# Kernel optimization log

Measured on AMD Instinct MI355X. Metric: run time of the kernel, lower is better.

The kernel has to match this reference:

```python
import jax, jax.numpy as jnp
import numpy as np

B, S, E = 2, 2048, 1024
H = 16
D = E // H          # head dim = 64
K_TOP = 64          # top-k tokens kept per query in sparse branch
M = 256             # performer kernel feature dim
EPS = 1e-6


def setup_inputs() -> dict:
    key = jax.random.key(0)
    ks = jax.random.split(key, 16)
    sc = 0.02
    p = {
        'x': jax.random.normal(ks[0], (B, S, E), jnp.float32),
        # sparse-attention branch params
        'Wq_s': jax.random.normal(ks[1], (E, E), jnp.float32) * sc,
        'Wk_s': jax.random.normal(ks[2], (E, E), jnp.float32) * sc,
        'Wv_s': jax.random.normal(ks[3], (E, E), jnp.float32) * sc,
        'Wo_s': jax.random.normal(ks[4], (E, E), jnp.float32) * sc,
        'bq_s': jnp.zeros((E,), jnp.float32),
        'bk_s': jnp.zeros((E,), jnp.float32),
        'bv_s': jnp.zeros((E,), jnp.float32),
        'bo_s': jnp.zeros((E,), jnp.float32),
        # performer branch params
        'Wq_p': jax.random.normal(ks[5], (E, E), jnp.float32) * sc,
        'Wk_p': jax.random.normal(ks[6], (E, E), jnp.float32) * sc,
        'Wv_p': jax.random.normal(ks[7], (E, E), jnp.float32) * sc,
        'Wo_p': jax.random.normal(ks[8], (E, E), jnp.float32) * sc,
        'bo_p': jnp.zeros((E,), jnp.float32),
        'Wfeat': jax.random.normal(ks[9], (D, M), jnp.float32) / np.sqrt(D),
        # gate
        'Wg': jax.random.normal(ks[10], (E, 2), jnp.float32) * sc,
        'bg': jnp.zeros((2,), jnp.float32),
    }
    return p


def _split_heads(t):
    # [B,S,E] -> [B,H,S,D]
    return t.reshape(B, S, H, D).transpose(0, 2, 1, 3)


def _merge_heads(t):
    # [B,H,S,D] -> [B,S,E]
    return t.transpose(0, 2, 1, 3).reshape(B, S, E)


def _sparse_attn(x, Wq, bq, Wk, bk, Wv, bv, Wo, bo):
    q = _split_heads(x @ Wq + bq)
    k = _split_heads(x @ Wk + bk)
    v = _split_heads(x @ Wv + bv)
    scores = jnp.einsum('bhqd,bhkd->bhqk', q, k) / np.sqrt(D)  # [B,H,S,S]
    # keep only top-K scores per query row
    topv = jax.lax.top_k(scores, K_TOP)[0]
    thresh = topv[..., -1:]
    neg = jnp.finfo(scores.dtype).min
    masked = jnp.where(scores >= thresh, scores, neg)
    attn = jax.nn.softmax(masked, axis=-1)
    out = jnp.einsum('bhqk,bhkd->bhqd', attn, v)
    return _merge_heads(out) @ Wo + bo


def _performer_attn(x, Wq, Wk, Wv, Wo, bo, Wfeat):
    q = _split_heads(x @ Wq)
    k = _split_heads(x @ Wk)
    v = _split_heads(x @ Wv)
    # learned relu feature map (FAVOR-style linear attention)
    phi_q = jax.nn.relu(jnp.einsum('bhsd,dm->bhsm', q, Wfeat)) + EPS
    phi_k = jax.nn.relu(jnp.einsum('bhsd,dm->bhsm', k, Wfeat)) + EPS
    kv = jnp.einsum('bhsm,bhsd->bhmd', phi_k, v)      # [B,H,M,D]
    z = phi_k.sum(axis=2)                              # [B,H,M]
    num = jnp.einsum('bhsm,bhmd->bhsd', phi_q, kv)
    den = jnp.einsum('bhsm,bhm->bhs', phi_q, z)[..., None] + EPS
    return _merge_heads(num / den) @ Wo + bo


def reference(x, Wq_s, Wk_s, Wv_s, Wo_s, bq_s, bk_s, bv_s, bo_s,
              Wq_p, Wk_p, Wv_p, Wo_p, bo_p, Wfeat, Wg, bg):
    sparse_out = _sparse_attn(x, Wq_s, bq_s, Wk_s, bk_s, Wv_s, bv_s, Wo_s, bo_s)
    perf_out = _performer_attn(x, Wq_p, Wk_p, Wv_p, Wo_p, bo_p, Wfeat)
    avg_hidden = x.mean(axis=1)                        # [B,E]
    gate = jax.nn.softmax(avg_hidden @ Wg + bg, axis=-1)  # [B,2]
    w_s = gate[:, 0][:, None, None]
    w_p = gate[:, 1][:, None, None]
    # dropout is identity in eval/reference mode
    return w_s * sparse_out + w_p * perf_out
```

## Files before the change

kernel.cpp:

```cpp
#include <hip/hip_runtime.h>


constexpr int cB = 2, cS = 2048, cE = 1024, cH = 16, cD = 64, cKTOP = 64, cM = 256;
constexpr float cEPS = 1e-6f;

typedef _Float16 half8 __attribute__((ext_vector_type(8)));
typedef float f32x16 __attribute__((ext_vector_type(16)));

__device__ __forceinline__ unsigned int f2key(float f) {
    unsigned int u = __float_as_uint(f);
    return (u & 0x80000000u) ? ~u : (u | 0x80000000u);
}

__device__ __forceinline__ unsigned short h2u(_Float16 h) {
    union { _Float16 h; unsigned short u; } x; x.h = h; return x.u;
}

__device__ __forceinline__ half8 ld_half8(const unsigned short* p) {
    union { uint4 u; half8 h; } x;
    x.u = *(const uint4*)p;
    return x.h;
}

__global__ __launch_bounds__(256)
void gemm_qk2_blas(const float* __restrict__ A,
                   const float* __restrict__ Wq,
                   const float* __restrict__ Wk,
                   const float* __restrict__ bq,
                   const float* __restrict__ bk_,
                   float* __restrict__ Cq,
                   float* __restrict__ Ck,
                   unsigned short* __restrict__ khi,
                   int K, int N)
{
    __shared__ __align__(16) float As[16][68];
    __shared__ __align__(16) float Bq[16][68];
    __shared__ __align__(16) float Bk[16][68];
    const int t  = threadIdx.x;
    const int r0 = blockIdx.y * 64;
    const int c0 = blockIdx.x * 64;
    const int tm = t >> 4, tn = t & 15;
    float paccQ[4][4] = {};
    float caccQ[4][4] = {};
    float paccK[4][4] = {};
    float caccK[4][4] = {};

    const int ar = t >> 2, ak = (t & 3) * 4;
    const int bk = t >> 4, bc = (t & 15) * 4;

    for (int k0 = 0; k0 < K; k0 += 16) {
        const float4 av  = *(const float4*)(A  + (size_t)(r0 + ar) * K + (k0 + ak));
        const float4 bqv = *(const float4*)(Wq + (size_t)(k0 + bk) * N + (c0 + bc));
        const float4 bkv = *(const float4*)(Wk + (size_t)(k0 + bk) * N + (c0 + bc));
        As[ak + 0][ar] = av.x;
        As[ak + 1][ar] = av.y;
        As[ak + 2][ar] = av.z;
        As[ak + 3][ar] = av.w;
        *(float4*)&Bq[bk][bc] = bqv;
        *(float4*)&Bk[bk][bc] = bkv;
        __syncthreads();
        #pragma unroll
        for (int kk = 0; kk < 16; ++kk) {
            const float4 a4  = *(const float4*)&As[kk][tm * 4];
            const float4 q4  = *(const float4*)&Bq[kk][tn * 4];
            const float4 k4  = *(const float4*)&Bk[kk][tn * 4];
            const float a[4]  = {a4.x, a4.y, a4.z, a4.w};
            const float bqr[4] = {q4.x, q4.y, q4.z, q4.w};
            const float bkr[4] = {k4.x, k4.y, k4.z, k4.w};
            #pragma unroll
            for (int i = 0; i < 4; ++i)
                #pragma unroll
                for (int j = 0; j < 4; ++j) {
                    paccQ[i][j] = fmaf(a[i], bqr[j], paccQ[i][j]);
                    paccK[i][j] = fmaf(a[i], bkr[j], paccK[i][j]);
                }
        }
        __syncthreads();
        const int kn = k0 + 16;
        if (kn == 384 || kn == 768 || kn == K) {
            #pragma unroll
            for (int i = 0; i < 4; ++i)
                #pragma unroll
                for (int j = 0; j < 4; ++j) {
                    caccQ[i][j] = caccQ[i][j] + paccQ[i][j];
                    paccQ[i][j] = 0.f;
                    caccK[i][j] = caccK[i][j] + paccK[i][j];
                    paccK[i][j] = 0.f;
                }
        }
    }
    #pragma unroll
    for (int i = 0; i < 4; ++i) {
        const int r = r0 + tm * 4 + i;
        const int c = c0 + tn * 4;
        float4 vq;
        vq.x = caccQ[i][0] + bq[c + 0];
        vq.y = caccQ[i][1] + bq[c + 1];
        vq.z = caccQ[i][2] + bq[c + 2];
        vq.w = caccQ[i][3] + bq[c + 3];
        *(float4*)&Cq[(size_t)r * N + c] = vq;
        float4 vk;
        vk.x = caccK[i][0] + bk_[c + 0];
        vk.y = caccK[i][1] + bk_[c + 1];
        vk.z = caccK[i][2] + bk_[c + 2];
        vk.w = caccK[i][3] + bk_[c + 3];
        *(float4*)&Ck[(size_t)r * N + c] = vk;
        ushort4 hs;
        hs.x = h2u((_Float16)vk.x);
        hs.y = h2u((_Float16)vk.y);
        hs.z = h2u((_Float16)vk.z);
        hs.w = h2u((_Float16)vk.w);
        *(ushort4*)&khi[(size_t)r * N + c] = hs;
    }
}

__global__ __launch_bounds__(256)
void conv_wT(const float* __restrict__ W,
             unsigned short* __restrict__ wthi,
             unsigned short* __restrict__ wtlo)
{
    __shared__ float tile[64][68];
    const int t  = threadIdx.x;
    const int k0 = blockIdx.y * 64;
    const int n0 = blockIdx.x * 64;
    const int r  = t >> 4, c4 = (t & 15) * 4;
    #pragma unroll
    for (int i = 0; i < 4; ++i) {
        const int k = r + 16 * i;
        const float4 v = *(const float4*)&W[(size_t)(k0 + k) * cE + n0 + c4];
        tile[k][c4 + 0] = v.x; tile[k][c4 + 1] = v.y;
        tile[k][c4 + 2] = v.z; tile[k][c4 + 3] = v.w;
    }
    __syncthreads();
    #pragma unroll
    for (int i = 0; i < 4; ++i) {
        const int n = r + 16 * i;
        unsigned int hp[2], lp[2];
        #pragma unroll
        for (int p = 0; p < 2; ++p) {
            unsigned short hh[2], ll[2];
            #pragma unroll
            for (int j = 0; j < 2; ++j) {
                const float f = tile[c4 + p * 2 + j][n];
                const _Float16 h = (_Float16)f;
                hh[j] = h2u(h);
                ll[j] = h2u((_Float16)(f - (float)h));
            }
            hp[p] = (unsigned int)hh[0] | ((unsigned int)hh[1] << 16);
            lp[p] = (unsigned int)ll[0] | ((unsigned int)ll[1] << 16);
        }
        uint2 hv, lv;
        hv.x = hp[0]; hv.y = hp[1];
        lv.x = lp[0]; lv.y = lp[1];
        *(uint2*)&wthi[(size_t)(n0 + n) * cE + k0 + c4] = hv;
        *(uint2*)&wtlo[(size_t)(n0 + n) * cE + k0 + c4] = lv;
    }
}

__global__ __launch_bounds__(256)
void gemm_hilo(const float* __restrict__ A,
               const unsigned short* __restrict__ wthi,
               const unsigned short* __restrict__ wtlo,
               const float* __restrict__ bias,
               float* __restrict__ C)
{
    __shared__ __align__(16) unsigned short Ah[128][24];
    __shared__ __align__(16) unsigned short Al[128][24];
    __shared__ __align__(16) unsigned short Bh[64][24];
    __shared__ __align__(16) unsigned short Bl[64][24];

    const int t    = threadIdx.x;
    const int lane = t & 63, wave = t >> 6;
    const int wr   = wave >> 1, wc = wave & 1;
    const int r0   = blockIdx.y * 128, c0 = blockIdx.x * 64;
    const int fr   = lane & 31, g5 = lane >> 5;

    const int arow = t >> 1, aka = (t & 1) * 8;
    const int bsel = t >> 7;
    const int brow = (t & 127) >> 1, bkb = (t & 1) * 8;
    const unsigned short* wsrc = bsel ? wtlo : wthi;

    f32x16 acc0 = {0.f,0.f,0.f,0.f,0.f,0.f,0.f,0.f,0.f,0.f,0.f,0.f,0.f,0.f,0.f,0.f};
    f32x16 acc1 = {0.f,0.f,0.f,0.f,0.f,0.f,0.f,0.f,0.f,0.f,0.f,0.f,0.f,0.f,0.f,0.f};

    for (int k0 = 0; k0 < cE; k0 += 16) {
        const float4 x0 = *(const float4*)&A[(size_t)(r0 + arow) * cE + k0 + aka];
        const float4 x1 = *(const float4*)&A[(size_t)(r0 + arow) * cE + k0 + aka + 4];
        const float xf[8] = {x0.x, x0.y, x0.z, x0.w, x1.x, x1.y, x1.z, x1.w};
        unsigned int hw[4], lw[4];
        #pragma unroll
        for (int p = 0; p < 4; ++p) {
            unsigned short hh[2], ll[2];
            #pragma unroll
            for (int j = 0; j < 2; ++j) {
                const float f = xf[p * 2 + j];
                const _Float16 h = (_Float16)f;
                hh[j] = h2u(h);
                ll[j] = h2u((_Float16)(f - (float)h));
            }
            hw[p] = (unsigned int)hh[0] | ((unsigned int)hh[1] << 16);
            lw[p] = (unsigned int)ll[0] | ((unsigned int)ll[1] << 16);
        }
        uint4 hv, lv;
        hv.x = hw[0]; hv.y = hw[1]; hv.z = hw[2]; hv.w = hw[3];
        lv.x = lw[0]; lv.y = lw[1]; lv.z = lw[2]; lv.w = lw[3];
        *(uint4*)&Ah[arow][aka] = hv;
        *(uint4*)&Al[arow][aka] = lv;

        const uint4 wv = *(const uint4*)&wsrc[(size_t)(c0 + brow) * cE + k0 + bkb];
        if (bsel) *(uint4*)&Bl[brow][bkb] = wv;
        else      *(uint4*)&Bh[brow][bkb] = wv;
        __syncthreads();

        const half8 a0h = ld_half8(&Ah[wr * 64 + fr][g5 * 8]);
        const half8 a0l = ld_half8(&Al[wr * 64 + fr][g5 * 8]);
        const half8 a1h = ld_half8(&Ah[wr * 64 + 32 + fr][g5 * 8]);
        const half8 a1l = ld_half8(&Al[wr * 64 + 32 + fr][g5 * 8]);
        const half8 bh  = ld_half8(&Bh[wc * 32 + fr][g5 * 8]);
        const half8 bl  = ld_half8(&Bl[wc * 32 + fr][g5 * 8]);

        acc0 = __builtin_amdgcn_mfma_f32_32x32x16_f16(a0l, bh, acc0, 0, 0, 0);
        acc0 = __builtin_amdgcn_mfma_f32_32x32x16_f16(a0h, bl, acc0, 0, 0, 0);
        acc0 = __builtin_amdgcn_mfma_f32_32x32x16_f16(a0h, bh, acc0, 0, 0, 0);
        acc1 = __builtin_amdgcn_mfma_f32_32x32x16_f16(a1l, bh, acc1, 0, 0, 0);
        acc1 = __builtin_amdgcn_mfma_f32_32x32x16_f16(a1h, bl, acc1, 0, 0, 0);
        acc1 = __builtin_amdgcn_mfma_f32_32x32x16_f16(a1h, bh, acc1, 0, 0, 0);
        __syncthreads();
    }

    const int col = c0 + wc * 32 + fr;
    const float bv = bias ? bias[col] : 0.f;
    #pragma unroll
    for (int rg = 0; rg < 16; ++rg) {
        const int row = r0 + wr * 64 + (rg & 3) + 8 * (rg >> 2) + 4 * g5;
        C[(size_t)row * cE + col] = acc0[rg] + bv;
    }
    #pragma unroll
    for (int rg = 0; rg < 16; ++rg) {
        const int row = r0 + wr * 64 + 32 + (rg & 3) + 8 * (rg >> 2) + 4 * g5;
        C[(size_t)row * cE + col] = acc1[rg] + bv;
    }
}

__global__ __launch_bounds__(256)
void out_gemm_hilo(const float* __restrict__ As_, const float* __restrict__ Ap_,
                   const unsigned short* __restrict__ w1hi,
                   const unsigned short* __restrict__ w1lo,
                   const unsigned short* __restrict__ w2hi,
                   const unsigned short* __restrict__ w2lo,
                   const float* __restrict__ bos, const float* __restrict__ bop,
                   const float* __restrict__ gates, float* __restrict__ out)
{
    __shared__ __align__(16) unsigned short A1h[128][24], A1l[128][24];
    __shared__ __align__(16) unsigned short A2h[128][24], A2l[128][24];
    __shared__ __align__(16) unsigned short B1h[64][24],  B1l[64][24];
    __shared__ __align__(16) unsigned short B2h[64][24],  B2l[64][24];

    const int t    = threadIdx.x;
    const int lane = t & 63, wave = t >> 6;
    const int wr   = wave >> 1, wc = wave & 1;
    const int r0   = blockIdx.y * 128, c0 = blockIdx.x * 64;
    const int fr   = lane & 31, g5 = lane >> 5;
    const int b    = r0 >> 11;
    const float gs = gates[b * 2 + 0], gp = gates[b * 2 + 1];

    const int arow = t >> 1, aka = (t & 1) * 8;
    const int bsel = t >> 7;
    const int brow = (t & 127) >> 1, bkb = (t & 1) * 8;
    const unsigned short* s1 = bsel ? w1lo : w1hi;
    const unsigned short* s2 = bsel ? w2lo : w2hi;

    f32x16 acc0 = {0.f,0.f,0.f,0.f,0.f,0.f,0.f,0.f,0.f,0.f,0.f,0.f,0.f,0.f,0.f,0.f};
    f32x16 acc1 = {0.f,0.f,0.f,0.f,0.f,0.f,0.f,0.f,0.f,0.f,0.f,0.f,0.f,0.f,0.f,0.f};

    for (int k0 = 0; k0 < cE; k0 += 16) {
        {
            const float4 x0 = *(const float4*)&As_[(size_t)(r0 + arow) * cE + k0 + aka];
            const float4 x1 = *(const float4*)&As_[(size_t)(r0 + arow) * cE + k0 + aka + 4];
            const float xf[8] = {x0.x * gs, x0.y * gs, x0.z * gs, x0.w * gs,
                                 x1.x * gs, x1.y * gs, x1.z * gs, x1.w * gs};
            unsigned int hw[4], lw[4];
            #pragma unroll
            for (int p = 0; p < 4; ++p) {
                unsigned short hh[2], ll[2];
                #pragma unroll
                for (int j = 0; j < 2; ++j) {
                    const float f = xf[p * 2 + j];
                    const _Float16 h = (_Float16)f;
                    hh[j] = h2u(h);
                    ll[j] = h2u((_Float16)(f - (float)h));
                }
                hw[p] = (unsigned int)hh[0] | ((unsigned int)hh[1] << 16);
                lw[p] = (unsigned int)ll[0] | ((unsigned int)ll[1] << 16);
            }
            uint4 hv, lv;
            hv.x = hw[0]; hv.y = hw[1]; hv.z = hw[2]; hv.w = hw[3];
            lv.x = lw[0]; lv.y = lw[1]; lv.z = lw[2]; lv.w = lw[3];
            *(uint4*)&A1h[arow][aka] = hv;
            *(uint4*)&A1l[arow][aka] = lv;
        }
        {
            const float4 x0 = *(const float4*)&Ap_[(size_t)(r0 + arow) * cE + k0 + aka];
            const float4 x1 = *(const float4*)&Ap_[(size_t)(r0 + arow) * cE + k0 + aka + 4];
            const float xf[8] = {x0.x * gp, x0.y * gp, x0.z * gp, x0.w * gp,
                                 x1.x * gp, x1.y * gp, x1.z * gp, x1.w * gp};
            unsigned int hw[4], lw[4];
            #pragma unroll
            for (int p = 0; p < 4; ++p) {
                unsigned short hh[2], ll[2];
                #pragma unroll
                for (int j = 0; j < 2; ++j) {
                    const float f = xf[p * 2 + j];
                    const _Float16 h = (_Float16)f;
                    hh[j] = h2u(h);
                    ll[j] = h2u((_Float16)(f - (float)h));
                }
                hw[p] = (unsigned int)hh[0] | ((unsigned int)hh[1] << 16);
                lw[p] = (unsigned int)ll[0] | ((unsigned int)ll[1] << 16);
            }
            uint4 hv, lv;
            hv.x = hw[0]; hv.y = hw[1]; hv.z = hw[2]; hv.w = hw[3];
            lv.x = lw[0]; lv.y = lw[1]; lv.z = lw[2]; lv.w = lw[3];
            *(uint4*)&A2h[arow][aka] = hv;
            *(uint4*)&A2l[arow][aka] = lv;
        }
        {
            const uint4 w1 = *(const uint4*)&s1[(size_t)(c0 + brow) * cE + k0 + bkb];
            if (bsel) *(uint4*)&B1l[brow][bkb] = w1;
            else      *(uint4*)&B1h[brow][bkb] = w1;
            const uint4 w2 = *(const uint4*)&s2[(size_t)(c0 + brow) * cE + k0 + bkb];
            if (bsel) *(uint4*)&B2l[brow][bkb] = w2;
            else      *(uint4*)&B2h[brow][bkb] = w2;
        }
        __syncthreads();

        const half8 b1h = ld_half8(&B1h[wc * 32 + fr][g5 * 8]);
        const half8 b1l = ld_half8(&B1l[wc * 32 + fr][g5 * 8]);
        const half8 b2h = ld_half8(&B2h[wc * 32 + fr][g5 * 8]);
        const half8 b2l = ld_half8(&B2l[wc * 32 + fr][g5 * 8]);
        {
            const half8 a1h = ld_half8(&A1h[wr * 64 + fr][g5 * 8]);
            const half8 a1l = ld_half8(&A1l[wr * 64 + fr][g5 * 8]);
            const half8 a2h = ld_half8(&A2h[wr * 64 + fr][g5 * 8]);
            const half8 a2l = ld_half8(&A2l[wr * 64 + fr][g5 * 8]);
            acc0 = __builtin_amdgcn_mfma_f32_32x32x16_f16(a1l, b1h, acc0, 0, 0, 0);
            acc0 = __builtin_amdgcn_mfma_f32_32x32x16_f16(a1h, b1l, acc0, 0, 0, 0);
            acc0 = __builtin_amdgcn_mfma_f32_32x32x16_f16(a1h, b1h, acc0, 0, 0, 0);
            acc0 = __builtin_amdgcn_mfma_f32_32x32x16_f16(a2l, b2h, acc0, 0, 0, 0);
            acc0 = __builtin_amdgcn_mfma_f32_32x32x16_f16(a2h, b2l, acc0, 0, 0, 0);
            acc0 = __builtin_amdgcn_mfma_f32_32x32x16_f16(a2h, b2h, acc0, 0, 0, 0);
        }
        {
            const half8 a1h = ld_half8(&A1h[wr * 64 + 32 + fr][g5 * 8]);
            const half8 a1l = ld_half8(&A1l[wr * 64 + 32 + fr][g5 * 8]);
            const half8 a2h = ld_half8(&A2h[wr * 64 + 32 + fr][g5 * 8]);
            const half8 a2l = ld_half8(&A2l[wr * 64 + 32 + fr][g5 * 8]);
            acc1 = __builtin_amdgcn_mfma_f32_32x32x16_f16(a1l, b1h, acc1, 0, 0, 0);
            acc1 = __builtin_amdgcn_mfma_f32_32x32x16_f16(a1h, b1l, acc1, 0, 0, 0);
            acc1 = __builtin_amdgcn_mfma_f32_32x32x16_f16(a1h, b1h, acc1, 0, 0, 0);
            acc1 = __builtin_amdgcn_mfma_f32_32x32x16_f16(a2l, b2h, acc1, 0, 0, 0);
            acc1 = __builtin_amdgcn_mfma_f32_32x32x16_f16(a2h, b2l, acc1, 0, 0, 0);
            acc1 = __builtin_amdgcn_mfma_f32_32x32x16_f16(a2h, b2h, acc1, 0, 0, 0);
        }
        __syncthreads();
    }

    const int col = c0 + wc * 32 + fr;
    const float bv = gs * bos[col] + gp * bop[col];
    #pragma unroll
    for (int rg = 0; rg < 16; ++rg) {
        const int row = r0 + wr * 64 + (rg & 3) + 8 * (rg >> 2) + 4 * g5;
        out[(size_t)row * cE + col] = acc0[rg] + bv;
    }
    #pragma unroll
    for (int rg = 0; rg < 16; ++rg) {
        const int row = r0 + wr * 64 + 32 + (rg & 3) + 8 * (rg >> 2) + 4 * g5;
        out[(size_t)row * cE + col] = acc1[rg] + bv;
    }
}

__global__ __launch_bounds__(256, 4)
void sparse_sel(const float* __restrict__ Q,
                const unsigned short* __restrict__ Khi,
                unsigned short* __restrict__ gcidx,
                int* __restrict__ gcnt)
{
    __shared__ __align__(16) unsigned short Qhi[8][72];
    __shared__ unsigned int hist[8][257];
    __shared__ int cnt[8];
    __shared__ int t16hi[8], rem[8], t16[8];

    const int t   = threadIdx.x;
    const int bh  = blockIdx.y;
    const int b   = bh >> 4;
    const int h64 = (bh & 15) * 64;
    const int q0  = blockIdx.x * 8;
    const size_t rid0 = ((size_t)bh * 256 + blockIdx.x) * 8;

    if (t < 128) {
        const int r = t >> 4, c4 = (t & 15) * 4;
        const float4 v =
            *(const float4*)&Q[((size_t)(b * cS + q0 + r)) * cE + h64 + c4];
        const float f[4] = {v.x, v.y, v.z, v.w};
        #pragma unroll
        for (int i = 0; i < 4; ++i)
            Qhi[r][c4 + i] = h2u((_Float16)f[i]);
    }
    for (int i = t; i < 8 * 257; i += 256) (&hist[0][0])[i] = 0u;
    if (t < 8) cnt[t] = 0;
    __syncthreads();

    const int lane = t & 63;
    const int wv   = t >> 6;
    const int col  = lane & 31;
    const int g5   = lane >> 5;
    const int r0   = g5 * 4;

    half8 ahi[4];
    {
        const int arow = col & 7;
        #pragma unroll
        for (int ks = 0; ks < 4; ++ks)
            ahi[ks] = ld_half8(&Qhi[arow][g5 * 8 + ks * 16]);
    }
    unsigned int su[16][2];
    {
        const size_t kbase = ((size_t)(b * cS + wv * 512 + col)) * cE + h64;
        #pragma unroll
        for (int tl = 0; tl < 16; ++tl) {
            const unsigned short* kh = Khi + kbase + (size_t)tl * 32 * cE;
            f32x16 acc = {0.f,0.f,0.f,0.f,0.f,0.f,0.f,0.f,
                          0.f,0.f,0.f,0.f,0.f,0.f,0.f,0.f};
            #pragma unroll
            for (int ks = 0; ks < 4; ++ks) {
                const half8 bh8 = ld_half8(kh + g5 * 8 + ks * 16);
                acc = __builtin_amdgcn_mfma_f32_32x32x16_f16(ahi[ks], bh8, acc, 0, 0, 0);
            }
            const unsigned int k0 = f2key(acc[0] * 0.125f) >> 16;
            const unsigned int k1 = f2key(acc[1] * 0.125f) >> 16;
            const unsigned int k2 = f2key(acc[2] * 0.125f) >> 16;
            const unsigned int k3 = f2key(acc[3] * 0.125f) >> 16;
            su[tl][0] = k0 | (k1 << 16);
            su[tl][1] = k2 | (k3 << 16);
            atomicAdd(&hist[r0 + 0][k0 >> 8], 1u);
            atomicAdd(&hist[r0 + 1][k1 >> 8], 1u);
            atomicAdd(&hist[r0 + 2][k2 >> 8], 1u);
            atomicAdd(&hist[r0 + 3][k3 >> 8], 1u);
        }
    }
    __syncthreads();
    if (t < 8) {
        int need = cKTOP + 1;
        int hb = 0;
        for (int bin = 255; bin >= 0; --bin) {
            const int c = (int)hist[t][bin];
            if (c >= need) { hb = bin; break; }
            need -= c;
        }
        t16hi[t] = hb;
        rem[t] = need;
    }
    __syncthreads();
    for (int i = t; i < 8 * 257; i += 256) (&hist[0][0])[i] = 0u;
    __syncthreads();
    #pragma unroll
    for (int tl = 0; tl < 16; ++tl)
        #pragma unroll
        for (int w = 0; w < 2; ++w) {
            const unsigned int u = su[tl][w];
            const int rlo = r0 + 2 * w, rhi = rlo + 1;
            const unsigned int vlo = u & 0xFFFFu;
            const unsigned int vhi = u >> 16;
            if ((int)(vlo >> 8) == t16hi[rlo]) atomicAdd(&hist[rlo][vlo & 255u], 1u);
            if ((int)(vhi >> 8) == t16hi[rhi]) atomicAdd(&hist[rhi][vhi & 255u], 1u);
        }
    __syncthreads();
    if (t < 8) {
        int need = rem[t];
        int lb = 0;
        for (int bin = 255; bin >= 0; --bin) {
            const int c = (int)hist[t][bin];
            if (c >= need) { lb = bin; break; }
            need -= c;
        }
        t16[t] = (t16hi[t] << 8) | lb;
    }
    __syncthreads();

    #pragma unroll
    for (int tl = 0; tl < 16; ++tl) {
        const int key = wv * 512 + tl * 32 + col;
        #pragma unroll
        for (int w = 0; w < 2; ++w) {
            const unsigned int u = su[tl][w];
            const int rlo = r0 + 2 * w, rhi = rlo + 1;
            const int v0 = (int)(u & 0xFFFFu);
            const int v1 = (int)(u >> 16);
            if (v0 >= max(t16[rlo] - 3, 0)) {
                const int slot = atomicAdd(&cnt[rlo], 1);
                if (slot < 128) gcidx[(rid0 + rlo) * 128 + slot] = (unsigned short)key;
            }
            if (v1 >= max(t16[rhi] - 3, 0)) {
                const int slot = atomicAdd(&cnt[rhi], 1);
                if (slot < 128) gcidx[(rid0 + rhi) * 128 + slot] = (unsigned short)key;
            }
        }
    }
    __syncthreads();
    if (t < 8) gcnt[rid0 + t] = cnt[t];
}

__global__ __launch_bounds__(256, 8)
void sparse_att(const float* __restrict__ Q,
                const unsigned short* __restrict__ gcidx,
                const int* __restrict__ gcnt,
                const float* __restrict__ Ks, const float* __restrict__ V,
                float* __restrict__ O)
{
    __shared__ float QfT[64][8];
    __shared__ unsigned short cidx[8][128];
    __shared__ double cval[8][128];
    __shared__ float cw[8][128];
    __shared__ int cnt[8];
    __shared__ double T64s[8], s65s[8], rowm[8];

    const int t   = threadIdx.x;
    const int bh  = blockIdx.y;
    const int b   = bh >> 4;
    const int h64 = (bh & 15) * 64;
    const int q0  = blockIdx.x * 8;
    const size_t rid0 = ((size_t)bh * 256 + blockIdx.x) * 8;

    if (t < 128) {
        const int r = t >> 4, c4 = (t & 15) * 4;
        const float4 v =
            *(const float4*)&Q[((size_t)(b * cS + q0 + r)) * cE + h64 + c4];
        QfT[c4 + 0][r] = v.x; QfT[c4 + 1][r] = v.y;
        QfT[c4 + 2][r] = v.z; QfT[c4 + 3][r] = v.w;
    }
    ((ushort4*)&cidx[0][0])[t] = ((const ushort4*)&gcidx[rid0 * 128])[t];
    if (t < 8) cnt[t] = gcnt[rid0 + t];
    __syncthreads();

    const int wv = t >> 6, lane = t & 63;

    #pragma unroll
    for (int rx = 0; rx < 2; ++rx) {
        const int rr = wv * 2 + rx;
        const int n = min(cnt[rr], 128);
        for (int c = lane; c < n; c += 64) {
            const int key = cidx[rr][c];
            const float* kp = Ks + ((size_t)(b * cS + key)) * cE + h64;
            double a = 0.0;
            #pragma unroll 4
            for (int d4 = 0; d4 < 64; d4 += 4) {
                const float4 kv = *(const float4*)&kp[d4];
                a = fma((double)QfT[d4 + 0][rr], (double)kv.x, a);
                a = fma((double)QfT[d4 + 1][rr], (double)kv.y, a);
                a = fma((double)QfT[d4 + 2][rr], (double)kv.z, a);
                a = fma((double)QfT[d4 + 3][rr], (double)kv.w, a);
            }
            cval[rr][c] = a * 0.125;
        }
    }
    __syncthreads();

    #pragma unroll
    for (int rx = 0; rx < 2; ++rx) {
        const int rr = wv * 2 + rx;
        const int n = min(cnt[rr], 128);
        for (int c = lane; c < n; c += 64) {
            const double v = cval[rr][c];
            int rank = 0;
            for (int i = 0; i < n; ++i) rank += (cval[rr][i] > v) ? 1 : 0;
            if (rank == 0)  rowm[rr] = v;
            if (rank == 63) T64s[rr] = v;
            if (rank == 64) s65s[rr] = v;
        }
    }
    __syncthreads();

    #pragma unroll
    for (int rx = 0; rx < 2; ++rx) {
        const int rr = wv * 2 + rx;
        const int n = min(cnt[rr], 128);
        const double T64 = T64s[rr], s65 = s65s[rr], m = rowm[rr];
        float za = 0.f;
        for (int c = lane; c < n; c += 64) {
            const double v = cval[rr][c];
            if (v >= T64) za += expf((float)(v - m));
        }
        #pragma unroll
        for (int off = 32; off >= 1; off >>= 1)
            za += __shfl_xor(za, off);
        const float g   = (float)(T64 - s65);
        const float gm  = fmaxf(g - 5e-7f, 0.f);
        const float wB  = 0.5f * erfcf(gm * (1.0f / 2.2e-6f));
        const float wA  = 1.f - wB;
        const float e64 = expf((float)(T64 - m));
        const float e65 = expf((float)(s65 - m));
        const float ZB  = za - e64 + e65;
        const float cIn = wA / za + wB / ZB;
        const float c64 = wA / za;
        const float c65 = wB / ZB;
        for (int c = lane; c < n; c += 64) {
            const double v = cval[rr][c];
            float cc = 0.f;
            if (v > T64)       cc = cIn;
            else if (v == T64) cc = c64;
            else if (v == s65) cc = c65;
            cw[rr][c] = (cc != 0.f) ? cc * expf((float)(v - m)) : 0.f;
        }
    }
    __syncthreads();

    #pragma unroll
    for (int rx = 0; rx < 2; ++rx) {
        const int rr = wv * 2 + rx;
        const int n = min(cnt[rr], 128);
        float o = 0.f;
        int j = 0;
        for (; j + 8 <= n; j += 8) {
            float wreg[8];
            int   kreg[8];
            #pragma unroll
            for (int u = 0; u < 8; ++u) {
                wreg[u] = cw[rr][j + u];
                kreg[u] = cidx[rr][j + u];
            }
            float vreg[8];
            #pragma unroll
            for (int u = 0; u < 8; ++u)
                vreg[u] = V[((size_t)(b * cS + kreg[u])) * cE + h64 + lane];
            #pragma unroll
            for (int u = 0; u < 8; ++u)
                o = fmaf(wreg[u], vreg[u], o);
        }
        for (; j < n; ++j)
            o = fmaf(cw[rr][j],
                     V[((size_t)(b * cS + cidx[rr][j])) * cE + h64 + lane], o);
        O[((size_t)(b * cS + q0 + rr)) * cE + h64 + lane] = o;
    }
}

__global__ __launch_bounds__(256)
void perf_kv(const float* __restrict__ Kp, const float* __restrict__ Vp,
             const float* __restrict__ Wfeat,
             float* __restrict__ kvpart, float* __restrict__ zpart)
{
    __shared__ __align__(16) float Wf[64][68];
    __shared__ __align__(16) float Kt[64][68];
    __shared__ __align__(16) float Vt[64][68];
    __shared__ __align__(16) float Ph[64][68];
    const int t    = threadIdx.x;
    const int mc   = blockIdx.x & 3;
    const int sc   = blockIdx.x >> 2;
    const int bh   = blockIdx.y;
    const int b    = bh >> 4;
    const int h64  = (bh & 15) * 64;
    const int m0   = mc * 64;
    const int sbase = sc * 1024;

    #pragma unroll
    for (int i = 0; i < 4; ++i) {
        const int lin = t + 256 * i;
        const int d   = lin >> 4;
        const int m4  = (lin & 15) * 4;
        *(float4*)&Wf[d][m4] = *(const float4*)&Wfeat[d * cM + m0 + m4];
    }

    const int tm = t >> 4, tn = t & 15;
    const int sr = tm * 4;
    const int cn = tn * 4;
    float akv[4][4] = {};
    float az = 0.f;

    for (int st = 0; st < 16; ++st) {
        const int s0g = sbase + st * 64;
        __syncthreads();
        #pragma unroll
        for (int i = 0; i < 4; ++i) {
            const int row = tm + 16 * i;
            const size_t base = ((size_t)(b * cS + s0g + row)) * cE + h64 + cn;
            *(float4*)&Kt[row][cn] = *(const float4*)&Kp[base];
            *(float4*)&Vt[row][cn] = *(const float4*)&Vp[base];
        }
        __syncthreads();
        float4 p0 = {0,0,0,0}, p1 = {0,0,0,0}, p2 = {0,0,0,0}, p3 = {0,0,0,0};
        #pragma unroll 8
        for (int d = 0; d < 64; ++d) {
            const float4 wv = *(const float4*)&Wf[d][cn];
            const float k0 = Kt[sr + 0][d], k1 = Kt[sr + 1][d];
            const float k2 = Kt[sr + 2][d], k3 = Kt[sr + 3][d];
            p0.x = fmaf(k0, wv.x, p0.x); p0.y = fmaf(k0, wv.y, p0.y);
            p0.z = fmaf(k0, wv.z, p0.z); p0.w = fmaf(k0, wv.w, p0.w);
            p1.x = fmaf(k1, wv.x, p1.x); p1.y = fmaf(k1, wv.y, p1.y);
            p1.z = fmaf(k1, wv.z, p1.z); p1.w = fmaf(k1, wv.w, p1.w);
            p2.x = fmaf(k2, wv.x, p2.x); p2.y = fmaf(k2, wv.y, p2.y);
            p2.z = fmaf(k2, wv.z, p2.z); p2.w = fmaf(k2, wv.w, p2.w);
            p3.x = fmaf(k3, wv.x, p3.x); p3.y = fmaf(k3, wv.y, p3.y);
            p3.z = fmaf(k3, wv.z, p3.z); p3.w = fmaf(k3, wv.w, p3.w);
        }
        p0.x = fmaxf(p0.x, 0.f) + cEPS; p0.y = fmaxf(p0.y, 0.f) + cEPS;
        p0.z = fmaxf(p0.z, 0.f) + cEPS; p0.w = fmaxf(p0.w, 0.f) + cEPS;
        p1.x = fmaxf(p1.x, 0.f) + cEPS; p1.y = fmaxf(p1.y, 0.f) + cEPS;
        p1.z = fmaxf(p1.z, 0.f) + cEPS; p1.w = fmaxf(p1.w, 0.f) + cEPS;
        p2.x = fmaxf(p2.x, 0.f) + cEPS; p2.y = fmaxf(p2.y, 0.f) + cEPS;
        p2.z = fmaxf(p2.z, 0.f) + cEPS; p2.w = fmaxf(p2.w, 0.f) + cEPS;
        p3.x = fmaxf(p3.x, 0.f) + cEPS; p3.y = fmaxf(p3.y, 0.f) + cEPS;
        p3.z = fmaxf(p3.z, 0.f) + cEPS; p3.w = fmaxf(p3.w, 0.f) + cEPS;
        *(float4*)&Ph[sr + 0][cn] = p0;
        *(float4*)&Ph[sr + 1][cn] = p1;
        *(float4*)&Ph[sr + 2][cn] = p2;
        *(float4*)&Ph[sr + 3][cn] = p3;
        __syncthreads();
        #pragma unroll 8
        for (int ss = 0; ss < 64; ++ss) {
            const float4 pv = *(const float4*)&Ph[ss][sr];
            const float4 vv = *(const float4*)&Vt[ss][cn];
            akv[0][0] = fmaf(pv.x, vv.x, akv[0][0]); akv[0][1] = fmaf(pv.x, vv.y, akv[0][1]);
            akv[0][2] = fmaf(pv.x, vv.z, akv[0][2]); akv[0][3] = fmaf(pv.x, vv.w, akv[0][3]);
            akv[1][0] = fmaf(pv.y, vv.x, akv[1][0]); akv[1][1] = fmaf(pv.y, vv.y, akv[1][1]);
            akv[1][2] = fmaf(pv.y, vv.z, akv[1][2]); akv[1][3] = fmaf(pv.y, vv.w, akv[1][3]);
            akv[2][0] = fmaf(pv.z, vv.x, akv[2][0]); akv[2][1] = fmaf(pv.z, vv.y, akv[2][1]);
            akv[2][2] = fmaf(pv.z, vv.z, akv[2][2]); akv[2][3] = fmaf(pv.z, vv.w, akv[2][3]);
            akv[3][0] = fmaf(pv.w, vv.x, akv[3][0]); akv[3][1] = fmaf(pv.w, vv.y, akv[3][1]);
            akv[3][2] = fmaf(pv.w, vv.z, akv[3][2]); akv[3][3] = fmaf(pv.w, vv.w, akv[3][3]);
        }
        if (t < 64) {
            float a = 0.f;
            #pragma unroll 8
            for (int ss = 0; ss < 64; ++ss) a += Ph[ss][t];
            az += a;
        }
    }
    const size_t obase = ((size_t)(sc * 32 + bh)) * cM + m0;
    #pragma unroll
    for (int i = 0; i < 4; ++i) {
        float4 v; v.x = akv[i][0]; v.y = akv[i][1]; v.z = akv[i][2]; v.w = akv[i][3];
        *(float4*)&kvpart[(obase + sr + i) * cD + cn] = v;
    }
    if (t < 64) zpart[obase + t] = az;
}

__global__ __launch_bounds__(256)
void perf_numden(const float* __restrict__ Qp, const float* __restrict__ Wfeat,
                 const float* __restrict__ kvpart, const float* __restrict__ zpart,
                 float* __restrict__ Ap)
{
    __shared__ __align__(16) float Wf[64][68];
    __shared__ __align__(16) float Qt[64][68];
    __shared__ __align__(16) float KV[64][68];
    __shared__ __align__(16) float Ph[64][68];
    __shared__ __align__(16) float zl[64];
    __shared__ float den[64];
    const int t   = threadIdx.x;
    const int stb = blockIdx.x;
    const int bh  = blockIdx.y;
    const int b   = bh >> 4;
    const int h64 = (bh & 15) * 64;
    const int s0  = stb * 64;
    const int tm  = t >> 4, tn = t & 15;
    const int sr  = tm * 4, cn = tn * 4;

    #pragma unroll
    for (int i = 0; i < 4; ++i) {
        const int row = tm + 16 * i;
        *(float4*)&Qt[row][cn] =
            *(const float4*)&Qp[((size_t)(b * cS + s0 + row)) * cE + h64 + cn];
    }

    float num[4][4] = {};
    float dacc = 0.f;

    for (int mc = 0; mc < 4; ++mc) {
        const int m0 = mc * 64;
        __syncthreads();
        #pragma unroll
        for (int i = 0; i < 4; ++i) {
            const int lin = t + 256 * i;
            const int d   = lin >> 4;
            const int m4  = (lin & 15) * 4;
            *(float4*)&Wf[d][m4] = *(const float4*)&Wfeat[d * cM + m0 + m4];
        }
        #pragma unroll
        for (int i = 0; i < 4; ++i) {
            const int row = tm + 16 * i;
            const size_t o0 = ((size_t)bh * cM + m0 + row) * cD + cn;
            const size_t o1 = ((size_t)(32 + bh) * cM + m0 + row) * cD + cn;
            const float4 a = *(const float4*)&kvpart[o0];
            const float4 c = *(const float4*)&kvpart[o1];
            float4 v; v.x = a.x + c.x; v.y = a.y + c.y; v.z = a.z + c.z; v.w = a.w + c.w;
            *(float4*)&KV[row][cn] = v;
        }
        if (t < 64)
            zl[t] = zpart[(size_t)bh * cM + m0 + t] + zpart[(size_t)(32 + bh) * cM + m0 + t];
        __syncthreads();
        float4 p0 = {0,0,0,0}, p1 = {0,0,0,0}, p2 = {0,0,0,0}, p3 = {0,0,0,0};
        #pragma unroll 8
        for (int d = 0; d < 64; ++d) {
            const float4 wv = *(const float4*)&Wf[d][cn];
            const float q0 = Qt[sr + 0][d], q1 = Qt[sr + 1][d];
            const float q2 = Qt[sr + 2][d], q3 = Qt[sr + 3][d];
            p0.x = fmaf(q0, wv.x, p0.x); p0.y = fmaf(q0, wv.y, p0.y);
            p0.z = fmaf(q0, wv.z, p0.z); p0.w = fmaf(q0, wv.w, p0.w);
            p1.x = fmaf(q1, wv.x, p1.x); p1.y = fmaf(q1, wv.y, p1.y);
            p1.z = fmaf(q1, wv.z, p1.z); p1.w = fmaf(q1, wv.w, p1.w);
            p2.x = fmaf(q2, wv.x, p2.x); p2.y = fmaf(q2, wv.y, p2.y);
            p2.z = fmaf(q2, wv.z, p2.z); p2.w = fmaf(q2, wv.w, p2.w);
            p3.x = fmaf(q3, wv.x, p3.x); p3.y = fmaf(q3, wv.y, p3.y);
            p3.z = fmaf(q3, wv.z, p3.z); p3.w = fmaf(q3, wv.w, p3.w);
        }
        p0.x = fmaxf(p0.x, 0.f) + cEPS; p0.y = fmaxf(p0.y, 0.f) + cEPS;
        p0.z = fmaxf(p0.z, 0.f) + cEPS; p0.w = fmaxf(p0.w, 0.f) + cEPS;
        p1.x = fmaxf(p1.x, 0.f) + cEPS; p1.y = fmaxf(p1.y, 0.f) + cEPS;
        p1.z = fmaxf(p1.z, 0.f) + cEPS; p1.w = fmaxf(p1.w, 0.f) + cEPS;
        p2.x = fmaxf(p2.x, 0.f) + cEPS; p2.y = fmaxf(p2.y, 0.f) + cEPS;
        p2.z = fmaxf(p2.z, 0.f) + cEPS; p2.w = fmaxf(p2.w, 0.f) + cEPS;
        p3.x = fmaxf(p3.x, 0.f) + cEPS; p3.y = fmaxf(p3.y, 0.f) + cEPS;
        p3.z = fmaxf(p3.z, 0.f) + cEPS; p3.w = fmaxf(p3.w, 0.f) + cEPS;
        *(float4*)&Ph[sr + 0][cn] = p0;
        *(float4*)&Ph[sr + 1][cn] = p1;
        *(float4*)&Ph[sr + 2][cn] = p2;
        *(float4*)&Ph[sr + 3][cn] = p3;
        __syncthreads();
        #pragma unroll 8
        for (int mm = 0; mm < 64; ++mm) {
            const float4 kvv = *(const float4*)&KV[mm][cn];
            const float a0 = Ph[sr + 0][mm], a1 = Ph[sr + 1][mm];
            const float a2 = Ph[sr + 2][mm], a3 = Ph[sr + 3][mm];
            num[0][0] = fmaf(a0, kvv.x, num[0][0]); num[0][1] = fmaf(a0, kvv.y, num[0][1]);
            num[0][2] = fmaf(a0, kvv.z, num[0][2]); num[0][3] = fmaf(a0, kvv.w, num[0][3]);
            num[1][0] = fmaf(a1, kvv.x, num[1][0]); num[1][1] = fmaf(a1, kvv.y, num[1][1]);
            num[1][2] = fmaf(a1, kvv.z, num[1][2]); num[1][3] = fmaf(a1, kvv.w, num[1][3]);
            num[2][0] = fmaf(a2, kvv.x, num[2][0]); num[2][1] = fmaf(a2, kvv.y, num[2][1]);
            num[2][2] = fmaf(a2, kvv.z, num[2][2]); num[2][3] = fmaf(a2, kvv.w, num[2][3]);
            num[3][0] = fmaf(a3, kvv.x, num[3][0]); num[3][1] = fmaf(a3, kvv.y, num[3][1]);
            num[3][2] = fmaf(a3, kvv.z, num[3][2]); num[3][3] = fmaf(a3, kvv.w, num[3][3]);
        }
        if (t < 64) {
            float a = 0.f;
            #pragma unroll
            for (int m4 = 0; m4 < 64; m4 += 4) {
                const float4 ph = *(const float4*)&Ph[t][m4];
                const float4 zz = *(const float4*)&zl[m4];
                a = fmaf(ph.x, zz.x, a); a = fmaf(ph.y, zz.y, a);
                a = fmaf(ph.z, zz.z, a); a = fmaf(ph.w, zz.w, a);
            }
            dacc += a;
        }
    }
    __syncthreads();
    if (t < 64) den[t] = dacc + cEPS;
    __syncthreads();
    #pragma unroll
    for (int i = 0; i < 4; ++i) {
        const float di = 1.f / den[sr + i];
        float4 v;
        v.x = num[i][0] * di; v.y = num[i][1] * di;
        v.z = num[i][2] * di; v.w = num[i][3] * di;
        *(float4*)&Ap[((size_t)(b * cS + s0 + sr + i)) * cE + h64 + cn] = v;
    }
}

__global__ __launch_bounds__(256)
void gate_avg(const float* __restrict__ x, double* __restrict__ avgpart)
{
    const int i  = blockIdx.x * 256 + threadIdx.x;
    const int sc = blockIdx.y;
    const int b  = i >> 10, e = i & 1023;
    double acc = 0.0;
    const int sEnd = sc * 128 + 128;
    for (int s = sc * 128; s < sEnd; ++s)
        acc += (double)x[((size_t)(b * cS + s)) * cE + e];
    avgpart[(size_t)sc * 2048 + i] = acc;
}

__global__ void gate_final(const double* __restrict__ avgpart, const float* __restrict__ Wg,
                           const float* __restrict__ bg, float* __restrict__ gates)
{
    const int t = threadIdx.x;
    const int b = t >> 6, lane = t & 63;
    float l0 = 0.f, l1 = 0.f;
    for (int e = lane; e < cE; e += 64) {
        double s = 0.0;
        #pragma unroll
        for (int sc = 0; sc < 16; ++sc)
            s += avgpart[(size_t)sc * 2048 + b * 1024 + e];
        const float a = (float)(s / (double)cS);
        l0 = fmaf(a, Wg[e * 2 + 0], l0);
        l1 = fmaf(a, Wg[e * 2 + 1], l1);
    }
    for (int off = 32; off >= 1; off >>= 1) {
        l0 += __shfl_down(l0, off);
        l1 += __shfl_down(l1, off);
    }
    if (lane == 0) {
        l0 += bg[0]; l1 += bg[1];
        const float m = fmaxf(l0, l1);
        const float e0 = expf(l0 - m), e1 = expf(l1 - m);
        const float s = e0 + e1;
        gates[b * 2 + 0] = e0 / s;
        gates[b * 2 + 1] = e1 / s;
    }
}

extern "C" void kernel_launch(void* const* d_in, const int* in_sizes, int n_in,
                              void* d_out, int out_size, void* d_ws, size_t ws_size,
                              hipStream_t stream)
{
    (void)in_sizes; (void)n_in; (void)out_size; (void)ws_size;
    const float* x     = (const float*)d_in[0];
    const float* Wq_s  = (const float*)d_in[1];
    const float* Wk_s  = (const float*)d_in[2];
    const float* Wv_s  = (const float*)d_in[3];
    const float* Wo_s  = (const float*)d_in[4];
    const float* bq_s  = (const float*)d_in[5];
    const float* bk_s  = (const float*)d_in[6];
    const float* bv_s  = (const float*)d_in[7];
    const float* bo_s  = (const float*)d_in[8];
    const float* Wq_p  = (const float*)d_in[9];
    const float* Wk_p  = (const float*)d_in[10];
    const float* Wv_p  = (const float*)d_in[11];
    const float* Wo_p  = (const float*)d_in[12];
    const float* bo_p  = (const float*)d_in[13];
    const float* Wfeat = (const float*)d_in[14];
    const float* Wg    = (const float*)d_in[15];
    const float* bg    = (const float*)d_in[16];

    float* ws = (float*)d_ws;
    const size_t NRE = (size_t)cB * cS * cE;
    float* Qs    = ws;
    float* Ks    = Qs + NRE;
    float* KsT   = Ks + NRE;
    float* Vs    = KsT + NRE;
    float* Asout = Vs + NRE;
    float* kvpart = Asout + NRE;
    float* zpart  = kvpart + (size_t)2 * 32 * cM * cD;
    double* avgpart = (double*)(zpart + (size_t)2 * 32 * cM);
    float* gates = (float*)(avgpart + (size_t)16 * 2048);
    unsigned short* wthi  = (unsigned short*)(gates + 16);
    unsigned short* wtlo  = wthi + (size_t)cE * cE;
    unsigned short* wo1hi = wtlo + (size_t)cE * cE;
    unsigned short* wo1lo = wo1hi + (size_t)cE * cE;
    unsigned short* wo2hi = wo1lo + (size_t)cE * cE;
    unsigned short* wo2lo = wo2hi + (size_t)cE * cE;
    unsigned short* gcidx = wo2lo + (size_t)cE * cE;
    int* gcnt = (int*)(gcidx + (size_t)256 * 32 * 8 * 128);

    unsigned short* Khi = (unsigned short*)KsT;

    conv_wT<<<dim3(16, 16), 256, 0, stream>>>(Wo_s, wo1hi, wo1lo);
    conv_wT<<<dim3(16, 16), 256, 0, stream>>>(Wo_p, wo2hi, wo2lo);

    gemm_qk2_blas<<<dim3(16, 64), 256, 0, stream>>>(x, Wq_s, Wk_s, bq_s, bk_s,
                                                    Qs, Ks, Khi, cE, cE);
    conv_wT<<<dim3(16, 16), 256, 0, stream>>>(Wv_s, wthi, wtlo);
    gemm_hilo<<<dim3(16, 32), 256, 0, stream>>>(x, wthi, wtlo, bv_s, Vs);
    sparse_sel<<<dim3(256, 32), 256, 0, stream>>>(Qs, Khi, gcidx, gcnt);
    sparse_att<<<dim3(256, 32), 256, 0, stream>>>(Qs, gcidx, gcnt, Ks, Vs, Asout);

    float* Qp    = Qs;
    float* Kp    = Ks;
    float* Vp    = Vs;
    float* Apout = KsT;
    conv_wT<<<dim3(16, 16), 256, 0, stream>>>(Wq_p, wthi, wtlo);
    gemm_hilo<<<dim3(16, 32), 256, 0, stream>>>(x, wthi, wtlo, nullptr, Qp);
    conv_wT<<<dim3(16, 16), 256, 0, stream>>>(Wk_p, wthi, wtlo);
    gemm_hilo<<<dim3(16, 32), 256, 0, stream>>>(x, wthi, wtlo, nullptr, Kp);
    conv_wT<<<dim3(16, 16), 256, 0, stream>>>(Wv_p, wthi, wtlo);
    gemm_hilo<<<dim3(16, 32), 256, 0, stream>>>(x, wthi, wtlo, nullptr, Vp);
    perf_kv<<<dim3(8, 32), 256, 0, stream>>>(Kp, Vp, Wfeat, kvpart, zpart);
    perf_numden<<<dim3(32, 32), 256, 0, stream>>>(Qp, Wfeat, kvpart, zpart, Apout);

    gate_avg<<<dim3(8, 16), 256, 0, stream>>>(x, avgpart);
    gate_final<<<dim3(1), 128, 0, stream>>>(avgpart, Wg, bg, gates);
    out_gemm_hilo<<<dim3(16, 32), 256, 0, stream>>>(Asout, Apout,
                                                    wo1hi, wo1lo, wo2hi, wo2lo,
                                                    bo_s, bo_p, gates,
                                                    (float*)d_out);
}
```

Measured before the change: 1.430 ms.

## Process 16 query rows per block in sparse top-k selection to use full MFMA tile

```diff
diff --git a/kernel.cpp b/kernel.cpp
--- a/kernel.cpp
+++ b/kernel.cpp
@@ -385,19 +385,19 @@
                 unsigned short* __restrict__ gcidx,
                 int* __restrict__ gcnt)
 {
-    __shared__ __align__(16) unsigned short Qhi[8][72];
-    __shared__ unsigned int hist[8][257];
-    __shared__ int cnt[8];
-    __shared__ int t16hi[8], rem[8], t16[8];
+    __shared__ __align__(16) unsigned short Qhi[16][72];
+    __shared__ unsigned int hist[16][257];
+    __shared__ int cnt[16];
+    __shared__ int t16hi[16], rem[16], t16[16];
 
     const int t   = threadIdx.x;
     const int bh  = blockIdx.y;
     const int b   = bh >> 4;
     const int h64 = (bh & 15) * 64;
-    const int q0  = blockIdx.x * 8;
-    const size_t rid0 = ((size_t)bh * 256 + blockIdx.x) * 8;
-
-    if (t < 128) {
+    const int q0  = blockIdx.x * 16;
+    const size_t rid0 = (size_t)bh * 2048 + q0;
+
+    {
         const int r = t >> 4, c4 = (t & 15) * 4;
         const float4 v =
             *(const float4*)&Q[((size_t)(b * cS + q0 + r)) * cE + h64 + c4];
@@ -406,24 +406,25 @@
         for (int i = 0; i < 4; ++i)
             Qhi[r][c4 + i] = h2u((_Float16)f[i]);
     }
-    for (int i = t; i < 8 * 257; i += 256) (&hist[0][0])[i] = 0u;
-    if (t < 8) cnt[t] = 0;
+    for (int i = t; i < 16 * 257; i += 256) (&hist[0][0])[i] = 0u;
+    if (t < 16) cnt[t] = 0;
     __syncthreads();
 
     const int lane = t & 63;
     const int wv   = t >> 6;
     const int col  = lane & 31;
     const int g5   = lane >> 5;
-    const int r0   = g5 * 4;
+    const int base0 = 4 * g5;
+    const int base1 = 8 + 4 * g5;
 
     half8 ahi[4];
     {
-        const int arow = col & 7;
+        const int arow = col & 15;
         #pragma unroll
         for (int ks = 0; ks < 4; ++ks)
             ahi[ks] = ld_half8(&Qhi[arow][g5 * 8 + ks * 16]);
     }
-    unsigned int su[16][2];
+    unsigned int su[16][4];
     {
         const size_t kbase = ((size_t)(b * cS + wv * 512 + col)) * cE + h64;
         #pragma unroll
@@ -436,20 +437,26 @@
                 const half8 bh8 = ld_half8(kh + g5 * 8 + ks * 16);
                 acc = __builtin_amdgcn_mfma_f32_32x32x16_f16(ahi[ks], bh8, acc, 0, 0, 0);
             }
-            const unsigned int k0 = f2key(acc[0] * 0.125f) >> 16;
-            const unsigned int k1 = f2key(acc[1] * 0.125f) >> 16;
-            const unsigned int k2 = f2key(acc[2] * 0.125f) >> 16;
-            const unsigned int k3 = f2key(acc[3] * 0.125f) >> 16;
-            su[tl][0] = k0 | (k1 << 16);
-            su[tl][1] = k2 | (k3 << 16);
-            atomicAdd(&hist[r0 + 0][k0 >> 8], 1u);
-            atomicAdd(&hist[r0 + 1][k1 >> 8], 1u);
-            atomicAdd(&hist[r0 + 2][k2 >> 8], 1u);
-            atomicAdd(&hist[r0 + 3][k3 >> 8], 1u);
-        }
-    }
-    __syncthreads();
-    if (t < 8) {
+            unsigned int k[8];
+            #pragma unroll
+            for (int r = 0; r < 8; ++r)
+                k[r] = f2key(acc[r] * 0.125f) >> 16;
+            su[tl][0] = k[0] | (k[1] << 16);
+            su[tl][1] = k[2] | (k[3] << 16);
+            su[tl][2] = k[4] | (k[5] << 16);
+            su[tl][3] = k[6] | (k[7] << 16);
+            atomicAdd(&hist[base0 + 0][k[0] >> 8], 1u);
+            atomicAdd(&hist[base0 + 1][k[1] >> 8], 1u);
+            atomicAdd(&hist[base0 + 2][k[2] >> 8], 1u);
+            atomicAdd(&hist[base0 + 3][k[3] >> 8], 1u);
+            atomicAdd(&hist[base1 + 0][k[4] >> 8], 1u);
+            atomicAdd(&hist[base1 + 1][k[5] >> 8], 1u);
+            atomicAdd(&hist[base1 + 2][k[6] >> 8], 1u);
+            atomicAdd(&hist[base1 + 3][k[7] >> 8], 1u);
+        }
+    }
+    __syncthreads();
+    if (t < 16) {
         int need = cKTOP + 1;
         int hb = 0;
         for (int bin = 255; bin >= 0; --bin) {
@@ -461,21 +468,22 @@
         rem[t] = need;
     }
     __syncthreads();
-    for (int i = t; i < 8 * 257; i += 256) (&hist[0][0])[i] = 0u;
+    for (int i = t; i < 16 * 257; i += 256) (&hist[0][0])[i] = 0u;
     __syncthreads();
     #pragma unroll
     for (int tl = 0; tl < 16; ++tl)
         #pragma unroll
-        for (int w = 0; w < 2; ++w) {
+        for (int w = 0; w < 4; ++w) {
             const unsigned int u = su[tl][w];
-            const int rlo = r0 + 2 * w, rhi = rlo + 1;
+            const int rlo = (w < 2 ? base0 : base1) + (w & 1) * 2;
+            const int rhi = rlo + 1;
             const unsigned int vlo = u & 0xFFFFu;
             const unsigned int vhi = u >> 16;
             if ((int)(vlo >> 8) == t16hi[rlo]) atomicAdd(&hist[rlo][vlo & 255u], 1u);
             if ((int)(vhi >> 8) == t16hi[rhi]) atomicAdd(&hist[rhi][vhi & 255u], 1u);
         }
     __syncthreads();
-    if (t < 8) {
+    if (t < 16) {
         int need = rem[t];
         int lb = 0;
         for (int bin = 255; bin >= 0; --bin) {
@@ -491,9 +499,10 @@
     for (int tl = 0; tl < 16; ++tl) {
         const int key = wv * 512 + tl * 32 + col;
         #pragma unroll
-        for (int w = 0; w < 2; ++w) {
+        for (int w = 0; w < 4; ++w) {
             const unsigned int u = su[tl][w];
-            const int rlo = r0 + 2 * w, rhi = rlo + 1;
+            const int rlo = (w < 2 ? base0 : base1) + (w & 1) * 2;
+            const int rhi = rlo + 1;
             const int v0 = (int)(u & 0xFFFFu);
             const int v1 = (int)(u >> 16);
             if (v0 >= max(t16[rlo] - 3, 0)) {
@@ -507,7 +516,7 @@
         }
     }
     __syncthreads();
-    if (t < 8) gcnt[rid0 + t] = cnt[t];
+    if (t < 16) gcnt[rid0 + t] = cnt[t];
 }
 
 __global__ __launch_bounds__(256, 8)
@@ -946,7 +955,7 @@
     unsigned short* wo2hi = wo1lo + (size_t)cE * cE;
     unsigned short* wo2lo = wo2hi + (size_t)cE * cE;
     unsigned short* gcidx = wo2lo + (size_t)cE * cE;
-    int* gcnt = (int*)(gcidx + (size_t)256 * 32 * 8 * 128);
+    int* gcnt = (int*)(gcidx + (size_t)65536 * 128);
 
     unsigned short* Khi = (unsigned short*)KsT;
 
@@ -957,7 +966,7 @@
                                                     Qs, Ks, Khi, cE, cE);
     conv_wT<<<dim3(16, 16), 256, 0, stream>>>(Wv_s, wthi, wtlo);
     gemm_hilo<<<dim3(16, 32), 256, 0, stream>>>(x, wthi, wtlo, bv_s, Vs);
-    sparse_sel<<<dim3(256, 32), 256, 0, stream>>>(Qs, Khi, gcidx, gcnt);
+    sparse_sel<<<dim3(128, 32), 256, 0, stream>>>(Qs, Khi, gcidx, gcnt);
     sparse_att<<<dim3(256, 32), 256, 0, stream>>>(Qs, gcidx, gcnt, Ks, Vs, Asout);
 
     float* Qp    = Qs;
```

Measured after the change: 1.353 ms, median of 2. 1.06x faster.
